# Kernel tuning notes

Hardware: AMD Instinct MI355X
Metric: run time of the kernel (lower is better)

## Reference

```python
import jax, jax.numpy as jnp
import numpy as np

EPS = 1e-5

def gather_neighbour(pc, idx):
    # pc: [B,N,d], idx: [B,Q,k] -> [B,Q,k,d]
    return jax.vmap(lambda p, i: p[i])(pc, idx)

def rel_pos_encoding(q_xyz, src_xyz, idx):
    # q_xyz: [B,Q,3], src_xyz: [B,N,3], idx: [B,Q,k] -> [B,Q,k,10]
    nbr = gather_neighbour(src_xyz, idx)              # [B,Q,k,3]
    tile = q_xyz[:, :, None, :]                       # [B,Q,1,3]
    rel = tile - nbr                                  # [B,Q,k,3]
    dis = jnp.sqrt(jnp.sum(rel * rel, axis=-1, keepdims=True))
    tile_b = jnp.broadcast_to(tile, nbr.shape)
    return jnp.concatenate([dis, rel, tile_b, nbr], axis=-1)

def conv_bn_relu(x, W, g, b, m, v):
    # 1x1 conv (bias-free) + inference BatchNorm + ReLU; x: [B,Q,K,Cin], W: [Cout,Cin]
    y = jnp.einsum('bqkc,oc->bqko', x, W)
    y = (y - m) * (g * jax.lax.rsqrt(v + EPS)) + b
    return jax.nn.relu(y)

def att_pool(x, Wfc, Wm, g, b, m, v):
    # x: [B,Q,K,C] -> [B,Q,1,Cout]; softmax over neighbor axis K
    att = jnp.einsum('bqkc,oc->bqko', x, Wfc)
    att = jax.nn.softmax(att, axis=2)
    agg = jnp.sum(x * att, axis=2, keepdims=True)     # [B,Q,1,C]
    return conv_bn_relu(agg, Wm, g, b, m, v)

def setup_inputs() -> dict:
    key = jax.random.key(0)
    ks = jax.random.split(key, 40)
    B, Q, k, Nd, Ns = 2, 16384, 16, 4096, 16384
    dim_lb, dim_sc, dim_nl = 128, 64, 128
    d_mid = dim_lb + 10 - dim_sc   # 74
    d_att = dim_lb + 10            # 138
    f32 = jnp.float32
    inp = {}
    inp['features_lb'] = jax.random.normal(ks[0], (B, Q, k, dim_lb), f32)
    inp['features_sc'] = jax.random.normal(ks[1], (B, Q, k, dim_sc), f32)
    inp['NM_lb'] = jax.random.randint(ks[2], (B, Q, k), 0, Nd)
    inp['NM_sc'] = jax.random.randint(ks[3], (B, Q, k), 0, Ns)
    inp['coords_lb'] = jax.random.normal(ks[4], (B, Nd, 3), f32)
    inp['coords_sc'] = jax.random.normal(ks[5], (B, Ns, 3), f32)
    inp['coords_queries'] = jax.random.normal(ks[6], (B, Q, 3), f32)
    inp['NM_cl'] = jax.random.randint(ks[7], (B, Q, k), 0, Q)
    def bn(i, c):
        return (jax.random.uniform(ks[i], (c,), f32) + 0.5,
                jax.random.normal(ks[i + 1], (c,), f32) * 0.1,
                jax.random.normal(ks[i + 2], (c,), f32) * 0.1,
                jax.random.uniform(ks[i + 3], (c,), f32) + 0.5)
    inp['W_lb'] = jax.random.normal(ks[8], (10, 10), f32) * 0.3
    inp['g_lb'], inp['b_lb'], inp['m_lb'], inp['v_lb'] = bn(9, 10)
    inp['W_sc'] = jax.random.normal(ks[13], (d_mid, 10), f32) * 0.3
    inp['g_sc'], inp['b_sc'], inp['m_sc'], inp['v_sc'] = bn(14, d_mid)
    inp['W_fc1'] = jax.random.normal(ks[18], (d_att, d_att), f32) * 0.08
    inp['W_mlp1'] = jax.random.normal(ks[19], (dim_nl, d_att), f32) * 0.08
    inp['g1'], inp['b1'], inp['m1'], inp['v1'] = bn(20, dim_nl)
    inp['W_cl'] = jax.random.normal(ks[24], (10, 10), f32) * 0.3
    inp['g_cl'], inp['b_cl'], inp['m_cl'], inp['v_cl'] = bn(25, 10)
    inp['W_fc2'] = jax.random.normal(ks[29], (d_att, d_att), f32) * 0.08
    inp['W_mlp2'] = jax.random.normal(ks[30], (dim_nl, d_att), f32) * 0.08
    inp['g2'], inp['b2'], inp['m2'], inp['v2'] = bn(31, dim_nl)
    return inp

def reference(features_lb, features_sc, NM_lb, NM_sc, coords_lb, coords_sc,
              coords_queries, NM_cl,
              W_lb, g_lb, b_lb, m_lb, v_lb,
              W_sc, g_sc, b_sc, m_sc, v_sc,
              W_fc1, W_mlp1, g1, b1, m1, v1,
              W_cl, g_cl, b_cl, m_cl, v_cl,
              W_fc2, W_mlp2, g2, b2, m2, v2):
    # branch 1: layer-below
    rppe_lb = conv_bn_relu(rel_pos_encoding(coords_queries, coords_lb, NM_lb),
                           W_lb, g_lb, b_lb, m_lb, v_lb)          # [B,Q,k,10]
    # branch 2: skip connection
    rppe_sc = conv_bn_relu(rel_pos_encoding(coords_queries, coords_sc, NM_sc),
                           W_sc, g_sc, b_sc, m_sc, v_sc)          # [B,Q,k,74]
    locSE_lb = jnp.concatenate([rppe_lb, features_lb], axis=-1)   # [B,Q,k,138]
    locSE_sc = jnp.concatenate([rppe_sc, features_sc], axis=-1)   # [B,Q,k,138]
    f_hat = jnp.concatenate([locSE_lb, locSE_sc], axis=2)         # [B,Q,2k,138]
    f_tilde = att_pool(f_hat, W_fc1, W_mlp1, g1, b1, m1, v1)      # [B,Q,1,128]
    # second aggregation over current layer (num_agg > 1)
    rppe_cl = conv_bn_relu(rel_pos_encoding(coords_queries, coords_queries, NM_cl),
                           W_cl, g_cl, b_cl, m_cl, v_cl)          # [B,Q,k,10]
    f_cur = gather_neighbour(f_tilde[:, :, 0, :], NM_cl)          # [B,Q,k,128]
    locSE_cl = jnp.concatenate([rppe_cl, f_cur], axis=-1)         # [B,Q,k,138]
    f_tilde = att_pool(locSE_cl, W_fc2, W_mlp2, g2, b2, m2, v2)   # [B,Q,1,128]
    # match torch output layout [B, dim_nl, Q, 1]
    return jnp.transpose(f_tilde, (0, 3, 1, 2))
```

## Files before the change

### kernel.cpp

```cpp
#include <hip/hip_runtime.h>
#include <cmath>

#define EPSF 1e-5f
typedef unsigned int  uint32;
typedef unsigned short u16;
typedef __attribute__((ext_vector_type(8))) short bfrag;
typedef __attribute__((ext_vector_type(4))) float f32x4;

constexpr int Qn   = 16384;
constexpr int KS   = 168;
constexpr int PXS  = 40;
constexpr int Nd   = 4096;

constexpr int OFF_W1  = 0;
constexpr int OFF_WM1 = 23040;
constexpr int OFF_W2  = 43520;
constexpr int OFF_WM2 = 66560;
constexpr int OFF_WLB = 87040;
constexpr int OFF_WSC = 87552;
constexpr int OFF_WCL = 90112;
constexpr int END_W   = 90624;
constexpr int BN_LB = 0;
constexpr int BN_SC = 20;
constexpr int BN_CL = 168;
constexpr int BN_M1 = 188;
constexpr int BN_M2 = 444;
constexpr int BN_TOT = 700;
constexpr int OFF_FT  = END_W + 2 * BN_TOT;
constexpr int PREP_N  = END_W + BN_TOT;

__device__ __forceinline__ u16 f2b(float f) {
    uint32 u = __float_as_uint(f);
    uint32 r = (u + 0x7fffu + ((u >> 16) & 1u)) >> 16;
    return (u16)r;
}
__device__ __forceinline__ float b2f(u16 h) {
    return __uint_as_float(((uint32)h) << 16);
}
__device__ __forceinline__ uint32 cvtpk(float a, float b) {
    uint32 r;
    asm("v_cvt_pk_bf16_f32 %0, %1, %2" : "=v"(r) : "v"(a), "v"(b));
    return r;
}
__device__ __forceinline__ u16 cvt1(float a) { return (u16)cvtpk(a, a); }

__global__ __launch_bounds__(256) void prep_weights(
    const float* __restrict__ Wfc1, const float* __restrict__ Wmlp1,
    const float* __restrict__ Wfc2, const float* __restrict__ Wmlp2,
    const float* __restrict__ Wlb,  const float* __restrict__ Wsc,
    const float* __restrict__ Wcl,
    const float* __restrict__ g_lb, const float* __restrict__ b_lb,
    const float* __restrict__ m_lb, const float* __restrict__ v_lb,
    const float* __restrict__ g_sc, const float* __restrict__ b_sc,
    const float* __restrict__ m_sc, const float* __restrict__ v_sc,
    const float* __restrict__ g_cl, const float* __restrict__ b_cl,
    const float* __restrict__ m_cl, const float* __restrict__ v_cl,
    const float* __restrict__ g1, const float* __restrict__ b1,
    const float* __restrict__ m1, const float* __restrict__ v1,
    const float* __restrict__ g2, const float* __restrict__ b2,
    const float* __restrict__ m2, const float* __restrict__ v2,
    u16* __restrict__ ws16)
{
    int i = blockIdx.x * 256 + threadIdx.x;
    if (i >= PREP_N) return;
    if (i >= END_W) {
        int j = i - END_W;
        const float *g, *bb, *m, *v; int o2;
        if (j < BN_SC)      { g = g_lb; bb = b_lb; m = m_lb; v = v_lb; o2 = j - BN_LB; }
        else if (j < BN_CL) { g = g_sc; bb = b_sc; m = m_sc; v = v_sc; o2 = j - BN_SC; }
        else if (j < BN_M1) { g = g_cl; bb = b_cl; m = m_cl; v = v_cl; o2 = j - BN_CL; }
        else if (j < BN_M2) { g = g1;   bb = b1;   m = m1;   v = v1;   o2 = j - BN_M1; }
        else                { g = g2;   bb = b2;   m = m2;   v = v2;   o2 = j - BN_M2; }
        int o = o2 >> 1;
        float sc_ = g[o] * rsqrtf(v[o] + EPSF);
        ((float*)(ws16 + END_W))[j] = (o2 & 1) ? (bb[o] - m[o] * sc_) : sc_;
        return;
    }
    int lane = (i >> 3) & 63, jj = i & 7;
    int row16 = lane & 15;
    int kf = ((lane >> 4) << 3) + jj;
    float v = 0.f;
    if (i < OFF_WLB) {
        const float* src; int nrows; int idx;
        if (i < OFF_WM1)      { src = Wfc1;  nrows = 138; idx = i - OFF_W1; }
        else if (i < OFF_W2)  { src = Wmlp1; nrows = 128; idx = i - OFF_WM1; }
        else if (i < OFF_WM2) { src = Wfc2;  nrows = 138; idx = i - OFF_W2; }
        else                  { src = Wmlp2; nrows = 128; idx = i - OFF_WM2; }
        int t = idx >> 9, nt = t / 5, kt = t - nt * 5;
        int row = nt * 16 + row16;
        int kp  = kt * 32 + kf;
        int k   = (kp < 10) ? kp : kp - 2;
        if (row < nrows && kp < 140 && kp != 10 && kp != 11) v = src[row * 138 + k];
    } else {
        const float* src; int nrows; int idx;
        if (i < OFF_WSC)      { src = Wlb; nrows = 10; idx = i - OFF_WLB; }
        else if (i < OFF_WCL) { src = Wsc; nrows = 74; idx = i - OFF_WSC; }
        else                  { src = Wcl; nrows = 10; idx = i - OFF_WCL; }
        int t = idx >> 9;
        int row = t * 16 + row16;
        if (row < nrows && kf < 10) v = src[row * 10 + kf];
    }
    ws16[i] = f2b(v);
}

__device__ __forceinline__ void softmax32(
    const f32x4& a0, const f32x4& a1, int nt, int q,
    int lane, int lrow, int lgr, const u16* fh, u16* aggs)
{
    const int ch  = nt * 16 + lrow;
    const int chp = ch + (ch >= 10 ? 2 : 0);
    float mx = a0[0];
    #pragma unroll
    for (int r = 1; r < 4; ++r) mx = fmaxf(mx, a0[r]);
    #pragma unroll
    for (int r = 0; r < 4; ++r) mx = fmaxf(mx, a1[r]);
    mx = fmaxf(mx, __shfl_xor(mx, 16));
    mx = fmaxf(mx, __shfl_xor(mx, 32));
    float s = 0.f, num = 0.f;
    #pragma unroll
    for (int r = 0; r < 4; ++r) {
        float e = __expf(a0[r] - mx);
        s += e;
        num += e * b2f(fh[(q * 32 + lgr * 4 + r) * KS + chp]);
    }
    #pragma unroll
    for (int r = 0; r < 4; ++r) {
        float e = __expf(a1[r] - mx);
        s += e;
        num += e * b2f(fh[(q * 32 + 16 + lgr * 4 + r) * KS + chp]);
    }
    s   += __shfl_xor(s, 16);   s   += __shfl_xor(s, 32);
    num += __shfl_xor(num, 16); num += __shfl_xor(num, 32);
    if (lane < 16) aggs[q * 160 + chp] = cvt1((ch < 138) ? (num / s) : 0.f);
}

__device__ __forceinline__ void softmax16(
    const f32x4& a0, int nt, int q,
    int lane, int lrow, int lgr, const u16* fh, u16* aggs)
{
    const int ch  = nt * 16 + lrow;
    const int chp = ch + (ch >= 10 ? 2 : 0);
    float mx = a0[0];
    #pragma unroll
    for (int r = 1; r < 4; ++r) mx = fmaxf(mx, a0[r]);
    mx = fmaxf(mx, __shfl_xor(mx, 16));
    mx = fmaxf(mx, __shfl_xor(mx, 32));
    float s = 0.f, num = 0.f;
    #pragma unroll
    for (int r = 0; r < 4; ++r) {
        float e = __expf(a0[r] - mx);
        s += e;
        num += e * b2f(fh[(q * 16 + lgr * 4 + r) * KS + chp]);
    }
    s   += __shfl_xor(s, 16);   s   += __shfl_xor(s, 32);
    num += __shfl_xor(num, 16); num += __shfl_xor(num, 32);
    if (lane < 16) aggs[q * 160 + chp] = cvt1((ch < 138) ? (num / s) : 0.f);
}

__global__ __launch_bounds__(512, 4) void stage1(
    const float* __restrict__ feat_lb, const float* __restrict__ feat_sc,
    const int* __restrict__ nm_lb, const int* __restrict__ nm_sc,
    const float* __restrict__ c_lb, const float* __restrict__ c_sc,
    const float* __restrict__ c_q,
    u16* __restrict__ ws16)
{
    __shared__ __align__(16) u16 fhat[128 * KS];
    __shared__ __align__(16) u16 pxs[128 * PXS];
    u16* aggs = pxs;

    const int tid  = threadIdx.x;
    const int bq0  = blockIdx.x * 4;
    const int b    = bq0 >> 14;
    const int lane = tid & 63;
    const int w    = tid >> 6;
    const int lrow = lane & 15;
    const int lgr  = lane >> 4;

    const u16* W1t  = ws16 + OFF_W1;
    const u16* Wm1t = ws16 + OFF_WM1;
    const float* bn = (const float*)(ws16 + END_W);
    u16* ft = ws16 + OFF_FT;

    bfrag wb[5];
    #pragma unroll
    for (int kt = 0; kt < 5; ++kt)
        wb[kt] = *(const bfrag*)&W1t[(((w * 5) + kt) << 9) + (lane << 3)];

    const int qc = w >> 1, hc = w & 1;
    bfrag wcv[3];
    float2 bnv[3];
    if (hc == 0) {
        wcv[0] = *(const bfrag*)&ws16[OFF_WLB + (lane << 3)];
        wcv[1] = *(const bfrag*)&ws16[OFF_WSC + (lane << 3)];
        wcv[2] = *(const bfrag*)&ws16[OFF_WSC + 512 + (lane << 3)];
        bnv[0] = (lrow < 10) ? *(const float2*)&bn[BN_LB + lrow * 2] : float2{0.f, 0.f};
        bnv[1] = *(const float2*)&bn[BN_SC + lrow * 2];
        bnv[2] = *(const float2*)&bn[BN_SC + (16 + lrow) * 2];
    } else {
        #pragma unroll
        for (int t = 0; t < 3; ++t) {
            wcv[t] = *(const bfrag*)&ws16[OFF_WSC + ((2 + t) << 9) + (lane << 3)];
            int o = (2 + t) * 16 + lrow;
            bnv[t] = (o < 74) ? *(const float2*)&bn[BN_SC + o * 2] : float2{0.f, 0.f};
        }
    }

    {
        const float4* flb = (const float4*)(feat_lb + (size_t)bq0 * 2048);
        float4 r0[4];
        #pragma unroll
        for (int it = 0; it < 4; ++it) r0[it] = flb[tid + it * 512];
        const float4* fsc = (const float4*)(feat_sc + (size_t)bq0 * 1024);
        float4 r1[2];
        #pragma unroll
        for (int it = 0; it < 2; ++it) r1[it] = fsc[tid + it * 512];
        #pragma unroll
        for (int it = 0; it < 4; ++it) {
            int u = tid + it * 512;
            int q = u >> 9, rem = u & 511, r = rem >> 5, c4 = rem & 31;
            uint32* d = (uint32*)&fhat[(q * 32 + r) * KS + 12 + c4 * 4];
            d[0] = cvtpk(r0[it].x, r0[it].y); d[1] = cvtpk(r0[it].z, r0[it].w);
        }
        #pragma unroll
        for (int it = 0; it < 2; ++it) {
            int u = tid + it * 512;
            int q = u >> 8, rem = u & 255, r = rem >> 4, c4 = rem & 15;
            uint32* d = (uint32*)&fhat[(q * 32 + 16 + r) * KS + 76 + c4 * 4];
            d[0] = cvtpk(r1[it].x, r1[it].y); d[1] = cvtpk(r1[it].z, r1[it].w);
        }
        for (int u = tid; u < 128 * 15; u += 512) {
            int row = u / 15, jj = u - row * 15;
            uint32* base = (uint32*)((char*)fhat + row * 336);
            if (jj == 0) base[5] = 0u; else base[69 + jj] = 0u;
        }
    }
    if (tid < 128) {
        const int q = tid >> 5, r = tid & 31;
        const int bq = bq0 + q;
        const bool lb = r < 16;
        const int idx = lb ? nm_lb[bq * 16 + r] : nm_sc[bq * 16 + (r - 16)];
        const float* nb = lb ? (c_lb + ((size_t)b * Nd + idx) * 3)
                             : (c_sc + ((size_t)b * Qn + idx) * 3);
        const float qx = c_q[bq * 3 + 0], qy = c_q[bq * 3 + 1], qz = c_q[bq * 3 + 2];
        const float nx = nb[0], ny = nb[1], nz = nb[2];
        const float rx = qx - nx, ry = qy - ny, rz = qz - nz;
        const float dd = sqrtf(rx * rx + ry * ry + rz * rz);
        uint32* pw = (uint32*)&pxs[tid * PXS];
        pw[0] = cvtpk(dd, rx); pw[1] = cvtpk(ry, rz); pw[2] = cvtpk(qx, qy);
        pw[3] = cvtpk(qz, nx); pw[4] = cvtpk(ny, nz);
        #pragma unroll
        for (int z = 5; z < 16; ++z) pw[z] = 0u;
    }
    __syncthreads();

    const f32x4 zf = {0.f, 0.f, 0.f, 0.f};

    {
        bfrag pa1 = *(const bfrag*)&pxs[(qc * 32 + 16 + lrow) * PXS + lgr * 8];
        if (hc == 0) {
            bfrag pa0 = *(const bfrag*)&pxs[(qc * 32 + lrow) * PXS + lgr * 8];
            f32x4 c = __builtin_amdgcn_mfma_f32_16x16x32_bf16(pa0, wcv[0], zf, 0, 0, 0);
            if (lrow < 10) {
                #pragma unroll
                for (int r = 0; r < 4; ++r)
                    fhat[(qc * 32 + lgr * 4 + r) * KS + lrow] =
                        cvt1(fmaxf(c[r] * bnv[0].x + bnv[0].y, 0.f));
            }
            #pragma unroll
            for (int t = 1; t < 3; ++t) {
                f32x4 c2 = __builtin_amdgcn_mfma_f32_16x16x32_bf16(pa1, wcv[t], zf, 0, 0, 0);
                const int o  = (t - 1) * 16 + lrow;
                const int cp = (o < 10) ? o : o + 2;
                #pragma unroll
                for (int r = 0; r < 4; ++r)
                    fhat[(qc * 32 + 16 + lgr * 4 + r) * KS + cp] =
                        cvt1(fmaxf(c2[r] * bnv[t].x + bnv[t].y, 0.f));
            }
        } else {
            #pragma unroll
            for (int t = 0; t < 3; ++t) {
                f32x4 c2 = __builtin_amdgcn_mfma_f32_16x16x32_bf16(pa1, wcv[t], zf, 0, 0, 0);
                const int o = (2 + t) * 16 + lrow;
                if (o < 74) {
                    #pragma unroll
                    for (int r = 0; r < 4; ++r)
                        fhat[(qc * 32 + 16 + lgr * 4 + r) * KS + o + 2] =
                            cvt1(fmaxf(c2[r] * bnv[t].x + bnv[t].y, 0.f));
                }
            }
        }
    }
    __syncthreads();

    for (int q = 0; q < 4; ++q) {
        bfrag af[2][5];
        #pragma unroll
        for (int mt = 0; mt < 2; ++mt)
            #pragma unroll
            for (int kt = 0; kt < 5; ++kt)
                af[mt][kt] = *(const bfrag*)&fhat[(q * 32 + mt * 16 + lrow) * KS + kt * 32 + lgr * 8];

        f32x4 a0 = zf, a1 = zf;
        #pragma unroll
        for (int kt = 0; kt < 5; ++kt) {
            a0 = __builtin_amdgcn_mfma_f32_16x16x32_bf16(af[0][kt], wb[kt], a0, 0, 0, 0);
            a1 = __builtin_amdgcn_mfma_f32_16x16x32_bf16(af[1][kt], wb[kt], a1, 0, 0, 0);
        }
        softmax32(a0, a1, w, q, lane, lrow, lgr, fhat, aggs);

        if (w >= 4 && (w - 4) == q) {
            f32x4 e0 = zf, e1 = zf;
            #pragma unroll
            for (int kt = 0; kt < 5; ++kt) {
                bfrag b8 = *(const bfrag*)&W1t[((40 + kt) << 9) + (lane << 3)];
                e0 = __builtin_amdgcn_mfma_f32_16x16x32_bf16(af[0][kt], b8, e0, 0, 0, 0);
                e1 = __builtin_amdgcn_mfma_f32_16x16x32_bf16(af[1][kt], b8, e1, 0, 0, 0);
            }
            softmax32(e0, e1, 8, q, lane, lrow, lgr, fhat, aggs);
        }
    }
    if (w < 4) {
        if (lane < 2)       aggs[w * 160 + 10 + lane] = 0;
        else if (lane < 16) aggs[w * 160 + 144 + lane] = 0;
    }
    bfrag wm[5];
    #pragma unroll
    for (int kt = 0; kt < 5; ++kt)
        wm[kt] = *(const bfrag*)&Wm1t[(((w * 5) + kt) << 9) + (lane << 3)];
    __syncthreads();

    bfrag am[5];
    #pragma unroll
    for (int kt = 0; kt < 5; ++kt)
        am[kt] = *(const bfrag*)&aggs[lrow * 160 + kt * 32 + lgr * 8];
    f32x4 c = zf;
    #pragma unroll
    for (int kt = 0; kt < 5; ++kt)
        c = __builtin_amdgcn_mfma_f32_16x16x32_bf16(am[kt], wm[kt], c, 0, 0, 0);
    if (lgr == 0) {
        const int o = w * 16 + lrow;
        float2 p = *(const float2*)&bn[BN_M1 + o * 2];
        #pragma unroll
        for (int r = 0; r < 4; ++r)
            ft[(size_t)(bq0 + r) * 128 + o] = cvt1(fmaxf(c[r] * p.x + p.y, 0.f));
    }
}

__global__ __launch_bounds__(512, 4) void stage2(
    const int* __restrict__ nm_cl, const float* __restrict__ c_q,
    const u16* __restrict__ ws16, float* __restrict__ out)
{
    __shared__ __align__(16) u16 fhat[128 * KS];
    __shared__ __align__(16) u16 pxs[128 * PXS];
    u16* aggs = pxs;

    const int tid  = threadIdx.x;
    const int bq0  = blockIdx.x * 8;
    const int b    = bq0 >> 14;
    const int q0   = bq0 & (Qn - 1);
    const int lane = tid & 63;
    const int w    = tid >> 6;
    const int lrow = lane & 15;
    const int lgr  = lane >> 4;

    const u16* W2t  = ws16 + OFF_W2;
    const u16* Wm2t = ws16 + OFF_WM2;
    const float* bn = (const float*)(ws16 + END_W);
    const u16* ft   = ws16 + OFF_FT;

    bfrag wb[5];
    #pragma unroll
    for (int kt = 0; kt < 5; ++kt)
        wb[kt] = *(const bfrag*)&W2t[(((w * 5) + kt) << 9) + (lane << 3)];
    bfrag wcl = *(const bfrag*)&ws16[OFF_WCL + (lane << 3)];
    float2 bncl = (lrow < 10) ? *(const float2*)&bn[BN_CL + lrow * 2] : float2{0.f, 0.f};

    for (int u = tid; u < 128 * 15; u += 512) {
        int row = u / 15, jj = u - row * 15;
        uint32* base = (uint32*)((char*)fhat + row * 336);
        if (jj == 0) base[5] = 0u; else base[69 + jj] = 0u;
    }
    if (tid < 128) {
        const int q = tid >> 4, r = tid & 15;
        const int bq = bq0 + q;
        const int idx = nm_cl[bq * 16 + r];
        const float* nb = c_q + ((size_t)(b << 14) + idx) * 3;
        const float qx = c_q[bq * 3 + 0], qy = c_q[bq * 3 + 1], qz = c_q[bq * 3 + 2];
        const float nx = nb[0], ny = nb[1], nz = nb[2];
        const float rx = qx - nx, ry = qy - ny, rz = qz - nz;
        const float dd = sqrtf(rx * rx + ry * ry + rz * rz);
        uint32* pw = (uint32*)&pxs[tid * PXS];
        pw[0] = cvtpk(dd, rx); pw[1] = cvtpk(ry, rz); pw[2] = cvtpk(qx, qy);
        pw[3] = cvtpk(qz, nx); pw[4] = cvtpk(ny, nz);
        #pragma unroll
        for (int z = 5; z < 16; ++z) pw[z] = 0u;
    }
    for (int u = tid; u < 8192; u += 512) {
        int row = u >> 6, c2 = u & 63;
        int idx = nm_cl[bq0 * 16 + row];
        const uint32* srow = (const uint32*)(ft + (size_t)((b << 14) + idx) * 128);
        *(uint32*)&fhat[row * KS + 12 + c2 * 2] = srow[c2];
    }
    __syncthreads();

    const f32x4 zf = {0.f, 0.f, 0.f, 0.f};

    {
        bfrag pa = *(const bfrag*)&pxs[(w * 16 + lrow) * PXS + lgr * 8];
        f32x4 c = __builtin_amdgcn_mfma_f32_16x16x32_bf16(pa, wcl, zf, 0, 0, 0);
        if (lrow < 10) {
            #pragma unroll
            for (int r = 0; r < 4; ++r)
                fhat[(w * 16 + lgr * 4 + r) * KS + lrow] =
                    cvt1(fmaxf(c[r] * bncl.x + bncl.y, 0.f));
        }
    }
    __syncthreads();

    for (int q = 0; q < 8; ++q) {
        bfrag af[5];
        #pragma unroll
        for (int kt = 0; kt < 5; ++kt)
            af[kt] = *(const bfrag*)&fhat[(q * 16 + lrow) * KS + kt * 32 + lgr * 8];

        f32x4 a0 = zf;
        #pragma unroll
        for (int kt = 0; kt < 5; ++kt)
            a0 = __builtin_amdgcn_mfma_f32_16x16x32_bf16(af[kt], wb[kt], a0, 0, 0, 0);
        softmax16(a0, w, q, lane, lrow, lgr, fhat, aggs);

        if (q == w) {
            f32x4 e0 = zf;
            #pragma unroll
            for (int kt = 0; kt < 5; ++kt) {
                bfrag b8 = *(const bfrag*)&W2t[((40 + kt) << 9) + (lane << 3)];
                e0 = __builtin_amdgcn_mfma_f32_16x16x32_bf16(af[kt], b8, e0, 0, 0, 0);
            }
            softmax16(e0, 8, q, lane, lrow, lgr, fhat, aggs);
        }
    }
    if (lane < 2)       aggs[w * 160 + 10 + lane] = 0;
    else if (lane < 16) aggs[w * 160 + 144 + lane] = 0;
    bfrag wm[5];
    #pragma unroll
    for (int kt = 0; kt < 5; ++kt)
        wm[kt] = *(const bfrag*)&Wm2t[(((w * 5) + kt) << 9) + (lane << 3)];
    __syncthreads();

    bfrag am[5];
    #pragma unroll
    for (int kt = 0; kt < 5; ++kt)
        am[kt] = *(const bfrag*)&aggs[lrow * 160 + kt * 32 + lgr * 8];
    f32x4 c = zf;
    #pragma unroll
    for (int kt = 0; kt < 5; ++kt)
        c = __builtin_amdgcn_mfma_f32_16x16x32_bf16(am[kt], wm[kt], c, 0, 0, 0);
    if (lgr < 2) {
        const int o = w * 16 + lrow;
        float2 p = *(const float2*)&bn[BN_M2 + o * 2];
        #pragma unroll
        for (int r = 0; r < 4; ++r) {
            const int qloc = lgr * 4 + r;
            out[((size_t)(b * 128 + o) << 14) + q0 + qloc] = fmaxf(c[r] * p.x + p.y, 0.f);
        }
    }
}

extern "C" void kernel_launch(void* const* d_in, const int* in_sizes, int n_in,
                              void* d_out, int out_size, void* d_ws, size_t ws_size,
                              hipStream_t stream)
{
    const float* feat_lb = (const float*)d_in[0];
    const float* feat_sc = (const float*)d_in[1];
    const int*   nm_lb   = (const int*)d_in[2];
    const int*   nm_sc   = (const int*)d_in[3];
    const float* c_lb    = (const float*)d_in[4];
    const float* c_sc    = (const float*)d_in[5];
    const float* c_q     = (const float*)d_in[6];
    const int*   nm_cl   = (const int*)d_in[7];
    const float* W_lb = (const float*)d_in[8];
    const float* g_lb = (const float*)d_in[9];
    const float* b_lb = (const float*)d_in[10];
    const float* m_lb = (const float*)d_in[11];
    const float* v_lb = (const float*)d_in[12];
    const float* W_sc = (const float*)d_in[13];
    const float* g_sc = (const float*)d_in[14];
    const float* b_sc = (const float*)d_in[15];
    const float* m_sc = (const float*)d_in[16];
    const float* v_sc = (const float*)d_in[17];
    const float* W_fc1  = (const float*)d_in[18];
    const float* W_mlp1 = (const float*)d_in[19];
    const float* g1 = (const float*)d_in[20];
    const float* b1 = (const float*)d_in[21];
    const float* m1 = (const float*)d_in[22];
    const float* v1 = (const float*)d_in[23];
    const float* W_cl = (const float*)d_in[24];
    const float* g_cl = (const float*)d_in[25];
    const float* b_cl = (const float*)d_in[26];
    const float* m_cl = (const float*)d_in[27];
    const float* v_cl = (const float*)d_in[28];
    const float* W_fc2  = (const float*)d_in[29];
    const float* W_mlp2 = (const float*)d_in[30];
    const float* g2 = (const float*)d_in[31];
    const float* b2 = (const float*)d_in[32];
    const float* m2 = (const float*)d_in[33];
    const float* v2 = (const float*)d_in[34];

    u16* ws16 = (u16*)d_ws;
    float* out = (float*)d_out;

    hipLaunchKernelGGL(prep_weights, dim3((PREP_N + 255) / 256), dim3(256), 0, stream,
        W_fc1, W_mlp1, W_fc2, W_mlp2, W_lb, W_sc, W_cl,
        g_lb, b_lb, m_lb, v_lb, g_sc, b_sc, m_sc, v_sc,
        g_cl, b_cl, m_cl, v_cl, g1, b1, m1, v1, g2, b2, m2, v2, ws16);

    hipLaunchKernelGGL(stage1, dim3(2 * Qn / 4), dim3(512), 0, stream,
        feat_lb, feat_sc, nm_lb, nm_sc, c_lb, c_sc, c_q, ws16);

    hipLaunchKernelGGL(stage2, dim3(2 * Qn / 8), dim3(512), 0, stream,
        nm_cl, c_q, ws16, out);
}
```

Measured before the change: 230.8 us.

## Reassign attention work so each wave owns queries instead of output tiles

The attention-pooling stage in both kernels now has each wave own a query (or half its output tiles) and load its activation fragments from LDS once. It then loops over output-channel tiles, streaming weight fragments from global memory, where before each wave held one weight tile in registers and looped over all queries. The load imbalance from the extra ninth tile, previously done by a single wave per query, is spread more evenly. The aggregation buffer row stride also changes from 160 to 168, likely to cut LDS bank conflicts. In exchange, weight fragments are now re-read from global/L2 for every tile.

```diff
diff --git a/kernel.cpp b/kernel.cpp
--- a/kernel.cpp
+++ b/kernel.cpp
@@ -10,6 +10,7 @@
 constexpr int Qn   = 16384;
 constexpr int KS   = 168;
 constexpr int PXS  = 40;
+constexpr int AGS  = 168;
 constexpr int Nd   = 4096;
 
 constexpr int OFF_W1  = 0;
@@ -103,10 +104,21 @@
     ws16[i] = f2b(v);
 }
 
-__device__ __forceinline__ void softmax32(
-    const f32x4& a0, const f32x4& a1, int nt, int q,
+__device__ __forceinline__ void att_unit32(
+    int nt, int q, const bfrag (&af)[2][5], const u16* __restrict__ Wt,
     int lane, int lrow, int lgr, const u16* fh, u16* aggs)
 {
+    const f32x4 zf = {0.f, 0.f, 0.f, 0.f};
+    bfrag bf[5];
+    #pragma unroll
+    for (int kt = 0; kt < 5; ++kt)
+        bf[kt] = *(const bfrag*)&Wt[((nt * 5 + kt) << 9) + (lane << 3)];
+    f32x4 a0 = zf, a1 = zf;
+    #pragma unroll
+    for (int kt = 0; kt < 5; ++kt) {
+        a0 = __builtin_amdgcn_mfma_f32_16x16x32_bf16(af[0][kt], bf[kt], a0, 0, 0, 0);
+        a1 = __builtin_amdgcn_mfma_f32_16x16x32_bf16(af[1][kt], bf[kt], a1, 0, 0, 0);
+    }
     const int ch  = nt * 16 + lrow;
     const int chp = ch + (ch >= 10 ? 2 : 0);
     float mx = a0[0];
@@ -131,13 +143,22 @@
     }
     s   += __shfl_xor(s, 16);   s   += __shfl_xor(s, 32);
     num += __shfl_xor(num, 16); num += __shfl_xor(num, 32);
-    if (lane < 16) aggs[q * 160 + chp] = cvt1((ch < 138) ? (num / s) : 0.f);
-}
-
-__device__ __forceinline__ void softmax16(
-    const f32x4& a0, int nt, int q,
+    if (lane < 16) aggs[q * AGS + chp] = cvt1((ch < 138) ? (num / s) : 0.f);
+}
+
+__device__ __forceinline__ void att_unit16(
+    int nt, int q, const bfrag (&af)[5], const u16* __restrict__ Wt,
     int lane, int lrow, int lgr, const u16* fh, u16* aggs)
 {
+    const f32x4 zf = {0.f, 0.f, 0.f, 0.f};
+    bfrag bf[5];
+    #pragma unroll
+    for (int kt = 0; kt < 5; ++kt)
+        bf[kt] = *(const bfrag*)&Wt[((nt * 5 + kt) << 9) + (lane << 3)];
+    f32x4 a0 = zf;
+    #pragma unroll
+    for (int kt = 0; kt < 5; ++kt)
+        a0 = __builtin_amdgcn_mfma_f32_16x16x32_bf16(af[kt], bf[kt], a0, 0, 0, 0);
     const int ch  = nt * 16 + lrow;
     const int chp = ch + (ch >= 10 ? 2 : 0);
     float mx = a0[0];
@@ -154,7 +175,7 @@
     }
     s   += __shfl_xor(s, 16);   s   += __shfl_xor(s, 32);
     num += __shfl_xor(num, 16); num += __shfl_xor(num, 32);
-    if (lane < 16) aggs[q * 160 + chp] = cvt1((ch < 138) ? (num / s) : 0.f);
+    if (lane < 16) aggs[q * AGS + chp] = cvt1((ch < 138) ? (num / s) : 0.f);
 }
 
 __global__ __launch_bounds__(512, 4) void stage1(
@@ -175,21 +196,17 @@
     const int w    = tid >> 6;
     const int lrow = lane & 15;
     const int lgr  = lane >> 4;
+    const int q    = w >> 1;
+    const int h    = w & 1;
 
     const u16* W1t  = ws16 + OFF_W1;
     const u16* Wm1t = ws16 + OFF_WM1;
     const float* bn = (const float*)(ws16 + END_W);
     u16* ft = ws16 + OFF_FT;
 
-    bfrag wb[5];
-    #pragma unroll
-    for (int kt = 0; kt < 5; ++kt)
-        wb[kt] = *(const bfrag*)&W1t[(((w * 5) + kt) << 9) + (lane << 3)];
-
-    const int qc = w >> 1, hc = w & 1;
     bfrag wcv[3];
     float2 bnv[3];
-    if (hc == 0) {
+    if (h == 0) {
         wcv[0] = *(const bfrag*)&ws16[OFF_WLB + (lane << 3)];
         wcv[1] = *(const bfrag*)&ws16[OFF_WSC + (lane << 3)];
         wcv[2] = *(const bfrag*)&ws16[OFF_WSC + 512 + (lane << 3)];
@@ -217,15 +234,15 @@
         #pragma unroll
         for (int it = 0; it < 4; ++it) {
             int u = tid + it * 512;
-            int q = u >> 9, rem = u & 511, r = rem >> 5, c4 = rem & 31;
-            uint32* d = (uint32*)&fhat[(q * 32 + r) * KS + 12 + c4 * 4];
+            int qq = u >> 9, rem = u & 511, r = rem >> 5, c4 = rem & 31;
+            uint32* d = (uint32*)&fhat[(qq * 32 + r) * KS + 12 + c4 * 4];
             d[0] = cvtpk(r0[it].x, r0[it].y); d[1] = cvtpk(r0[it].z, r0[it].w);
         }
         #pragma unroll
         for (int it = 0; it < 2; ++it) {
             int u = tid + it * 512;
-            int q = u >> 8, rem = u & 255, r = rem >> 4, c4 = rem & 15;
-            uint32* d = (uint32*)&fhat[(q * 32 + 16 + r) * KS + 76 + c4 * 4];
+            int qq = u >> 8, rem = u & 255, r = rem >> 4, c4 = rem & 15;
+            uint32* d = (uint32*)&fhat[(qq * 32 + 16 + r) * KS + 76 + c4 * 4];
             d[0] = cvtpk(r1[it].x, r1[it].y); d[1] = cvtpk(r1[it].z, r1[it].w);
         }
         for (int u = tid; u < 128 * 15; u += 512) {
@@ -235,8 +252,8 @@
         }
     }
     if (tid < 128) {
-        const int q = tid >> 5, r = tid & 31;
-        const int bq = bq0 + q;
+        const int qq = tid >> 5, r = tid & 31;
+        const int bq = bq0 + qq;
         const bool lb = r < 16;
         const int idx = lb ? nm_lb[bq * 16 + r] : nm_sc[bq * 16 + (r - 16)];
         const float* nb = lb ? (c_lb + ((size_t)b * Nd + idx) * 3)
@@ -256,14 +273,14 @@
     const f32x4 zf = {0.f, 0.f, 0.f, 0.f};
 
     {
-        bfrag pa1 = *(const bfrag*)&pxs[(qc * 32 + 16 + lrow) * PXS + lgr * 8];
-        if (hc == 0) {
-            bfrag pa0 = *(const bfrag*)&pxs[(qc * 32 + lrow) * PXS + lgr * 8];
+        bfrag pa1 = *(const bfrag*)&pxs[(q * 32 + 16 + lrow) * PXS + lgr * 8];
+        if (h == 0) {
+            bfrag pa0 = *(const bfrag*)&pxs[(q * 32 + lrow) * PXS + lgr * 8];
             f32x4 c = __builtin_amdgcn_mfma_f32_16x16x32_bf16(pa0, wcv[0], zf, 0, 0, 0);
             if (lrow < 10) {
                 #pragma unroll
                 for (int r = 0; r < 4; ++r)
-                    fhat[(qc * 32 + lgr * 4 + r) * KS + lrow] =
+                    fhat[(q * 32 + lgr * 4 + r) * KS + lrow] =
                         cvt1(fmaxf(c[r] * bnv[0].x + bnv[0].y, 0.f));
             }
             #pragma unroll
@@ -273,7 +290,7 @@
                 const int cp = (o < 10) ? o : o + 2;
                 #pragma unroll
                 for (int r = 0; r < 4; ++r)
-                    fhat[(qc * 32 + 16 + lgr * 4 + r) * KS + cp] =
+                    fhat[(q * 32 + 16 + lgr * 4 + r) * KS + cp] =
                         cvt1(fmaxf(c2[r] * bnv[t].x + bnv[t].y, 0.f));
             }
         } else {
@@ -284,7 +301,7 @@
                 if (o < 74) {
                     #pragma unroll
                     for (int r = 0; r < 4; ++r)
-                        fhat[(qc * 32 + 16 + lgr * 4 + r) * KS + o + 2] =
+                        fhat[(q * 32 + 16 + lgr * 4 + r) * KS + o + 2] =
                             cvt1(fmaxf(c2[r] * bnv[t].x + bnv[t].y, 0.f));
                 }
             }
@@ -292,36 +309,26 @@
     }
     __syncthreads();
 
-    for (int q = 0; q < 4; ++q) {
-        bfrag af[2][5];
-        #pragma unroll
-        for (int mt = 0; mt < 2; ++mt)
-            #pragma unroll
-            for (int kt = 0; kt < 5; ++kt)
-                af[mt][kt] = *(const bfrag*)&fhat[(q * 32 + mt * 16 + lrow) * KS + kt * 32 + lgr * 8];
-
-        f32x4 a0 = zf, a1 = zf;
-        #pragma unroll
-        for (int kt = 0; kt < 5; ++kt) {
-            a0 = __builtin_amdgcn_mfma_f32_16x16x32_bf16(af[0][kt], wb[kt], a0, 0, 0, 0);
-            a1 = __builtin_amdgcn_mfma_f32_16x16x32_bf16(af[1][kt], wb[kt], a1, 0, 0, 0);
-        }
-        softmax32(a0, a1, w, q, lane, lrow, lgr, fhat, aggs);
-
-        if (w >= 4 && (w - 4) == q) {
-            f32x4 e0 = zf, e1 = zf;
-            #pragma unroll
-            for (int kt = 0; kt < 5; ++kt) {
-                bfrag b8 = *(const bfrag*)&W1t[((40 + kt) << 9) + (lane << 3)];
-                e0 = __builtin_amdgcn_mfma_f32_16x16x32_bf16(af[0][kt], b8, e0, 0, 0, 0);
-                e1 = __builtin_amdgcn_mfma_f32_16x16x32_bf16(af[1][kt], b8, e1, 0, 0, 0);
-            }
-            softmax32(e0, e1, 8, q, lane, lrow, lgr, fhat, aggs);
-        }
-    }
-    if (w < 4) {
-        if (lane < 2)       aggs[w * 160 + 10 + lane] = 0;
-        else if (lane < 16) aggs[w * 160 + 144 + lane] = 0;
+    bfrag af[2][5];
+    #pragma unroll
+    for (int mt = 0; mt < 2; ++mt)
+        #pragma unroll
+        for (int kt = 0; kt < 5; ++kt)
+            af[mt][kt] = *(const bfrag*)&fhat[(q * 32 + mt * 16 + lrow) * KS + kt * 32 + lgr * 8];
+
+    if (h == 0) {
+        att_unit32(0, q, af, W1t, lane, lrow, lgr, fhat, aggs);
+        att_unit32(1, q, af, W1t, lane, lrow, lgr, fhat, aggs);
+        att_unit32(2, q, af, W1t, lane, lrow, lgr, fhat, aggs);
+        att_unit32(3, q, af, W1t, lane, lrow, lgr, fhat, aggs);
+        att_unit32(4, q, af, W1t, lane, lrow, lgr, fhat, aggs);
+        if (lane < 2)       aggs[q * AGS + 10 + lane] = 0;
+        else if (lane < 16) aggs[q * AGS + 144 + lane] = 0;
+    } else {
+        att_unit32(5, q, af, W1t, lane, lrow, lgr, fhat, aggs);
+        att_unit32(6, q, af, W1t, lane, lrow, lgr, fhat, aggs);
+        att_unit32(7, q, af, W1t, lane, lrow, lgr, fhat, aggs);
+        att_unit32(8, q, af, W1t, lane, lrow, lgr, fhat, aggs);
     }
     bfrag wm[5];
     #pragma unroll
@@ -332,7 +339,7 @@
     bfrag am[5];
     #pragma unroll
     for (int kt = 0; kt < 5; ++kt)
-        am[kt] = *(const bfrag*)&aggs[lrow * 160 + kt * 32 + lgr * 8];
+        am[kt] = *(const bfrag*)&aggs[lrow * AGS + kt * 32 + lgr * 8];
     f32x4 c = zf;
     #pragma unroll
     for (int kt = 0; kt < 5; ++kt)
@@ -368,10 +375,6 @@
     const float* bn = (const float*)(ws16 + END_W);
     const u16* ft   = ws16 + OFF_FT;
 
-    bfrag wb[5];
-    #pragma unroll
-    for (int kt = 0; kt < 5; ++kt)
-        wb[kt] = *(const bfrag*)&W2t[(((w * 5) + kt) << 9) + (lane << 3)];
     bfrag wcl = *(const bfrag*)&ws16[OFF_WCL + (lane << 3)];
     float2 bncl = (lrow < 10) ? *(const float2*)&bn[BN_CL + lrow * 2] : float2{0.f, 0.f};
 
@@ -381,8 +384,8 @@
         if (jj == 0) base[5] = 0u; else base[69 + jj] = 0u;
     }
     if (tid < 128) {
-        const int q = tid >> 4, r = tid & 15;
-        const int bq = bq0 + q;
+        const int qq = tid >> 4, r = tid & 15;
+        const int bq = bq0 + qq;
         const int idx = nm_cl[bq * 16 + r];
         const float* nb = c_q + ((size_t)(b << 14) + idx) * 3;
         const float qx = c_q[bq * 3 + 0], qy = c_q[bq * 3 + 1], qz = c_q[bq * 3 + 2];
@@ -417,30 +420,22 @@
     }
     __syncthreads();
 
-    for (int q = 0; q < 8; ++q) {
-        bfrag af[5];
-        #pragma unroll
-        for (int kt = 0; kt < 5; ++kt)
-            af[kt] = *(const bfrag*)&fhat[(q * 16 + lrow) * KS + kt * 32 + lgr * 8];
-
-        f32x4 a0 = zf;
-        #pragma unroll
-        for (int kt = 0; kt < 5; ++kt)
-            a0 = __builtin_amdgcn_mfma_f32_16x16x32_bf16(af[kt], wb[kt], a0, 0, 0, 0);
-        softmax16(a0, w, q, lane, lrow, lgr, fhat, aggs);
-
-        if (q == w) {
-            f32x4 e0 = zf;
-            #pragma unroll
-            for (int kt = 0; kt < 5; ++kt) {
-                bfrag b8 = *(const bfrag*)&W2t[((40 + kt) << 9) + (lane << 3)];
-                e0 = __builtin_amdgcn_mfma_f32_16x16x32_bf16(af[kt], b8, e0, 0, 0, 0);
-            }
-            softmax16(e0, 8, q, lane, lrow, lgr, fhat, aggs);
-        }
-    }
-    if (lane < 2)       aggs[w * 160 + 10 + lane] = 0;
-    else if (lane < 16) aggs[w * 160 + 144 + lane] = 0;
+    bfrag af[5];
+    #pragma unroll
+    for (int kt = 0; kt < 5; ++kt)
+        af[kt] = *(const bfrag*)&fhat[(w * 16 + lrow) * KS + kt * 32 + lgr * 8];
+
+    att_unit16(0, w, af, W2t, lane, lrow, lgr, fhat, aggs);
+    att_unit16(1, w, af, W2t, lane, lrow, lgr, fhat, aggs);
+    att_unit16(2, w, af, W2t, lane, lrow, lgr, fhat, aggs);
+    att_unit16(3, w, af, W2t, lane, lrow, lgr, fhat, aggs);
+    att_unit16(4, w, af, W2t, lane, lrow, lgr, fhat, aggs);
+    att_unit16(5, w, af, W2t, lane, lrow, lgr, fhat, aggs);
+    att_unit16(6, w, af, W2t, lane, lrow, lgr, fhat, aggs);
+    att_unit16(7, w, af, W2t, lane, lrow, lgr, fhat, aggs);
+    att_unit16(8, w, af, W2t, lane, lrow, lgr, fhat, aggs);
+    if (lane < 2)       aggs[w * AGS + 10 + lane] = 0;
+    else if (lane < 16) aggs[w * AGS + 144 + lane] = 0;
     bfrag wm[5];
     #pragma unroll
     for (int kt = 0; kt < 5; ++kt)
@@ -450,7 +445,7 @@
     bfrag am[5];
     #pragma unroll
     for (int kt = 0; kt < 5; ++kt)
-        am[kt] = *(const bfrag*)&aggs[lrow * 160 + kt * 32 + lgr * 8];
+        am[kt] = *(const bfrag*)&aggs[lrow * AGS + kt * 32 + lgr * 8];
     f32x4 c = zf;
     #pragma unroll
     for (int kt = 0; kt < 5; ++kt)
```

After: 257.2 us. 11.4% more time.
